# Kernel optimization log

Hardware: AMD Instinct MI355X
Metric: run time of the kernel (lower is better)

The kernel has to match this reference:

```python
import jax, jax.numpy as jnp
import numpy as np

B, S_IN, T_OUT, H, L, V = 64, 512, 64, 1024, 2, 1024


def setup_inputs() -> dict:
    key = jax.random.key(0)
    ks = iter(jax.random.split(key, 64))
    def p(shape, scale=0.02):
        return (jax.random.normal(next(ks), shape, jnp.float32) * scale)
    d = {"x": jax.random.normal(next(ks), (B, 2, S_IN), jnp.float32)}
    d["emb"] = p((V, H))
    for l in range(L):
        i = 2 if l == 0 else H
        d[f"enc_Wih{l}"] = p((3 * H, i)); d[f"enc_Whh{l}"] = p((3 * H, H))
        d[f"enc_bih{l}"] = p((3 * H,));   d[f"enc_bhh{l}"] = p((3 * H,))
        d[f"dec_Wih{l}"] = p((H, H));     d[f"dec_Whh{l}"] = p((H, H))
        d[f"dec_bih{l}"] = p((H,));       d[f"dec_bhh{l}"] = p((H,))
    d["hq_W"] = p((H, H)); d["hq_b"] = p((H,))
    d["comb_W"] = p((H, 2 * H)); d["comb_b"] = p((H,))
    d["fc_W"] = p((V, H)); d["fc_b"] = p((V,))
    return d


def _gru_layer(x_seq, Wih, Whh, bih, bhh):
    # x_seq: [B,T,I] -> (outputs [B,T,H], h_T [B,H]). PyTorch GRU gate order r,z,n.
    xp = jnp.einsum('bti,gi->btg', x_seq, Wih) + bih  # [B,T,3H]
    h0 = jnp.zeros((x_seq.shape[0], Whh.shape[1]), x_seq.dtype)
    def step(h, xpt):
        hp = h @ Whh.T + bhh
        xr, xz, xn = jnp.split(xpt, 3, axis=-1)
        hr, hz, hn = jnp.split(hp, 3, axis=-1)
        r = jax.nn.sigmoid(xr + hr)
        z = jax.nn.sigmoid(xz + hz)
        n = jnp.tanh(xn + r * hn)
        h = (1.0 - z) * n + z * h
        return h, h
    hT, ys = jax.lax.scan(step, h0, jnp.swapaxes(xp, 0, 1))
    return jnp.swapaxes(ys, 0, 1), hT


def _forward(x, emb,
             enc_Wih0, enc_Whh0, enc_bih0, enc_bhh0,
             enc_Wih1, enc_Whh1, enc_bih1, enc_bhh1,
             dec_Wih0, dec_Whh0, dec_bih0, dec_bhh0,
             dec_Wih1, dec_Whh1, dec_bih1, dec_bhh1,
             hq_W, hq_b, comb_W, comb_b, fc_W, fc_b):
    enc_params = [(enc_Wih0, enc_Whh0, enc_bih0, enc_bhh0),
                  (enc_Wih1, enc_Whh1, enc_bih1, enc_bhh1)]
    dec_params = [(dec_Wih0, dec_Whh0, dec_bih0, dec_bhh0),
                  (dec_Wih1, dec_Whh1, dec_bih1, dec_bhh1)]
    # ---- encoder: GRU over x permuted to [B, S_in, 2] ----
    seq = jnp.transpose(x, (0, 2, 1)).astype(jnp.float32)
    h_enc = []
    for (Wih, Whh, bih, bhh) in enc_params:
        seq, hT = _gru_layer(seq, Wih, Whh, bih, bhh)
        h_enc.append(hT)
    enc_outs = seq                      # [B, S_in, H]
    hidden0 = jnp.stack(h_enc, axis=0)  # [L, B, H]

    tok0 = jnp.zeros((B,), jnp.int32)
    def dec_step(carry, _):
        tok, hid = carry
        inp = emb[tok]                  # [B, H]
        new_h = []
        for l, (Wih, Whh, bih, bhh) in enumerate(dec_params):
            h = jnp.tanh(inp @ Wih.T + bih + hid[l] @ Whh.T + bhh)
            new_h.append(h)
            inp = h
        hid = jnp.stack(new_h, axis=0)
        q = inp @ hq_W.T + hq_b                          # [B, H]
        scores = jnp.einsum('bsh,bh->bs', enc_outs, q)   # [B, S_in]
        aw = jax.nn.softmax(scores, axis=1)
        att = jnp.einsum('bs,bsh->bh', aw, enc_outs)     # [B, H]
        logits = jnp.concatenate([inp, att], axis=-1) @ comb_W.T + comb_b
        logits = logits @ fc_W.T + fc_b                  # [B, V]
        tok = jnp.argmax(logits, axis=-1).astype(jnp.int32)
        return (tok, hid), (logits, aw)
    (_, hidden), (logits_t, aw_t) = jax.lax.scan(dec_step, (tok0, hidden0), None, length=T_OUT)
    vec_out = jnp.swapaxes(logits_t, 0, 1)   # [B, T_out, V]
    attn = aw_t[-1][:, None, :]              # [B, 1, S_in] (last step, as in source)
    return vec_out, hidden, attn


def reference(x, emb,
              enc_Wih0, enc_Whh0, enc_bih0, enc_bhh0,
              enc_Wih1, enc_Whh1, enc_bih1, enc_bhh1,
              dec_Wih0, dec_Whh0, dec_bih0, dec_bhh0,
              dec_Wih1, dec_Whh1, dec_bih1, dec_bhh1,
              hq_W, hq_b, comb_W, comb_b, fc_W, fc_b):
    return _forward(x, emb,
                    enc_Wih0, enc_Whh0, enc_bih0, enc_bhh0,
                    enc_Wih1, enc_Whh1, enc_bih1, enc_bhh1,
                    dec_Wih0, dec_Whh0, dec_bih0, dec_bhh0,
                    dec_Wih1, dec_Whh1, dec_bih1, dec_bhh1,
                    hq_W, hq_b, comb_W, comb_b, fc_W, fc_b)
```

## Files before the change

kernel.cpp:

```cpp
#include <hip/hip_runtime.h>
#include <stdint.h>


#define BB 64
#define SS 512
#define TT 64
#define HH 1024
#define VV 1024
#define BH 65536
#define SH 524288
#define OFF_HID  4194304
#define OFF_ATTN 4325376

typedef _Float16 half8  __attribute__((ext_vector_type(8)));
typedef float    floatx4 __attribute__((ext_vector_type(4)));

struct P {
  const float *x, *emb;
  const float *eWih0, *eWhh0, *ebih0, *ebhh0;
  const float *dWih0, *dWhh0, *dbih0, *dbhh0;
  const float *eWih1, *eWhh1, *ebih1, *ebhh1;
  const float *dWih1, *dWhh1, *dbih1, *dbhh1;
  const float *hqW, *hqb, *combW, *combb, *fcW, *fcb;
  uint32_t* enc_i;
  _Float16 *W0h,*W0l;
  _Float16 *W1h,*W1l;
  _Float16 *embh,*embl,*T0h,*T0l;
  _Float16 *wih0dh,*wih0dl,*wih1dh,*wih1dl,*whh0dh,*whh0dl,*whh1dh,*whh1dl;
  _Float16 *hqh,*hql,*combh,*combl,*fch,*fcl;
  _Float16 *h0h,*h0l,*h1h,*h1l;
  _Float16 *dh0h,*dh0l,*dh1h,*dh1l;
  _Float16 *cath,*catl;
  _Float16 *ch,*cl;
  float *u0,*u1,*w1x,*q;
  float *attp_o;
  float *attp_ml;
  float *sc63;
  unsigned long long* amax;
  float* dout;
};

struct GSet { const _Float16 *Wh, *Wl, *Ah, *Al; const float *bias; float *out; };

__device__ __forceinline__ void splitf(float x, _Float16& hi, _Float16& lo){
  _Float16 h = (_Float16)x; hi = h;
  lo = (_Float16)((x - (float)h) * 2048.0f);
}
__device__ __forceinline__ float reconf(_Float16 hi, _Float16 lo){
  return fmaf((float)lo, 1.0f/2048.0f, (float)hi);
}
__device__ __forceinline__ float recon_u32(uint32_t w){
  float hi = (float)__builtin_bit_cast(_Float16, (unsigned short)(w & 0xffffu));
  float lo = (float)__builtin_bit_cast(_Float16, (unsigned short)(w >> 16));
  return fmaf(lo, 1.0f/2048.0f, hi);
}
__device__ __forceinline__ uint32_t pack_pair(float x){
  _Float16 hi, lo; splitf(x, hi, lo);
  return (uint32_t)__builtin_bit_cast(unsigned short, hi)
       | ((uint32_t)__builtin_bit_cast(unsigned short, lo) << 16);
}
__device__ __forceinline__ unsigned ordf(float f){
  unsigned u = __float_as_uint(f);
  return (u & 0x80000000u) ? ~u : (u | 0x80000000u);
}

template<int NT, int KH, bool SPLIT>
__device__ __forceinline__ void gemm_core(
    const _Float16* __restrict__ Ah0, const _Float16* __restrict__ Al0,
    const _Float16* __restrict__ Ah1, const _Float16* __restrict__ Al1,
    int sA,
    const _Float16* __restrict__ Wh, const _Float16* __restrict__ Wl,
    int nrows, _Float16* ldsW, float* accOut)
{
  const int tid = threadIdx.x, lane = tid & 63, wave = tid >> 6;
  const int mA = (wave<<4) + (lane & 15);
  const int kb = ((lane>>4) << 3);
  const int wstride = KH << 10;
  floatx4 aH[NT], aM1[NT], aM2[NT];
  int ne[NT];
  const _Float16* bh_base[NT];
  const _Float16* bl_base[NT];
  #pragma unroll
  for (int nt=0; nt<NT; ++nt){
    int nn = (lane & 15) + (nt<<4);
    ne[nt] = nn < nrows ? nn : nrows - 1;
    bh_base[nt] = ldsW + ne[nt]*1032 + kb;
    aH[nt]  = floatx4{0.f,0.f,0.f,0.f};
    aM1[nt] = floatx4{0.f,0.f,0.f,0.f};
    aM2[nt] = floatx4{0.f,0.f,0.f,0.f};
  }
  #pragma unroll
  for (int kh=0; kh<KH; ++kh){
    __syncthreads();
    const int iters = (nrows*128 + 255) >> 8;
    for (int it=0; it<iters; ++it){
      int idx = tid + (it<<8);
      int row = idx >> 7, col = (idx & 127) << 3;
      if (row < nrows)
        *(half8*)(ldsW + row*1032 + col) =
            *(const half8*)(Wh + row*wstride + (kh<<10) + col);
    }
    __syncthreads();
    const _Float16* ah_p = ((KH==2 && kh==1) ? Ah1 : Ah0) + mA*sA + kb;
    const _Float16* al_p = ((KH==2 && kh==1) ? Al1 : Al0) + mA*sA + kb;
    #pragma unroll
    for (int nt=0; nt<NT; ++nt) bl_base[nt] = Wl + ne[nt]*wstride + (kh<<10) + kb;
    #pragma unroll 4
    for (int ks=0; ks<32; ++ks){
      half8 ah = *(const half8*)(ah_p + (ks<<5));
      half8 al = *(const half8*)(al_p + (ks<<5));
      #pragma unroll
      for (int nt=0; nt<NT; ++nt){
        half8 bh = *(const half8*)(bh_base[nt] + (ks<<5));
        half8 bl = *(const half8*)(bl_base[nt] + (ks<<5));
        aH[nt]  = __builtin_amdgcn_mfma_f32_16x16x32_f16(ah, bh, aH[nt],  0,0,0);
        aM1[nt] = __builtin_amdgcn_mfma_f32_16x16x32_f16(ah, bl, aM1[nt], 0,0,0);
        aM2[nt] = __builtin_amdgcn_mfma_f32_16x16x32_f16(al, bh, aM2[nt], 0,0,0);
      }
    }
    if (SPLIT){
      #pragma unroll
      for (int nt=0; nt<NT; ++nt){
        #pragma unroll
        for (int r=0;r<4;++r)
          accOut[(kh*NT + nt)*4 + r] = aH[nt][r] + (aM1[nt][r] + aM2[nt][r]) * (1.f/2048.f);
        aH[nt]  = floatx4{0.f,0.f,0.f,0.f};
        aM1[nt] = floatx4{0.f,0.f,0.f,0.f};
        aM2[nt] = floatx4{0.f,0.f,0.f,0.f};
      }
    }
  }
  if (!SPLIT){
    #pragma unroll
    for (int nt=0; nt<NT; ++nt)
      #pragma unroll
      for (int r=0;r<4;++r)
        accOut[nt*4 + r] = aH[nt][r] + (aM1[nt][r] + aM2[nt][r]) * (1.f/2048.f);
  }
}

__global__ __launch_bounds__(256) void k_split(const float* __restrict__ src,
                                               _Float16* dh, _Float16* dl, int n){
  for (int i = blockIdx.x*256 + threadIdx.x; i < n; i += gridDim.x*256){
    _Float16 hi,lo; splitf(src[i],hi,lo); dh[i]=hi; dl[i]=lo;
  }
}

__global__ __launch_bounds__(256) void k_rw0(P p){
  const int n = 128*24*1024;
  for (int i = blockIdx.x*256 + threadIdx.x; i < n; i += gridDim.x*256){
    int k = i & 1023; int rest = i >> 10; int rr = rest % 24; int blk = rest / 24;
    int grow = (rr>>3)*1024 + (blk<<3) + (rr&7);
    _Float16 hi,lo; splitf(p.eWhh0[grow*1024 + k],hi,lo);
    p.W0h[i]=hi; p.W0l[i]=lo;
  }
}
__global__ __launch_bounds__(256) void k_rw1(P p){
  const int n = 128*24*2048;
  for (int i = blockIdx.x*256 + threadIdx.x; i < n; i += gridDim.x*256){
    int k = i & 2047; int rest = i >> 11; int rr = rest % 24; int blk = rest / 24;
    int grow = (rr>>3)*1024 + (blk<<3) + (rr&7);
    float v = (k < 1024) ? p.eWhh1[grow*1024 + k] : p.eWih1[grow*1024 + (k-1024)];
    _Float16 hi,lo; splitf(v,hi,lo);
    p.W1h[i]=hi; p.W1l[i]=lo;
  }
}
__global__ __launch_bounds__(256) void k_zero(P p){
  int i = blockIdx.x*256 + threadIdx.x;
  p.h1h[i] = (_Float16)0.f; p.h1l[i] = (_Float16)0.f;
  p.h0h[BH + i] = (_Float16)0.f; p.h0l[BH + i] = (_Float16)0.f;
}
__global__ __launch_bounds__(256) void k_t0(P p){
  __shared__ _Float16 ldsW[16*1032];
  const int ns = blockIdx.x & 63, mc = blockIdx.x >> 6;
  float acc[4];
  gemm_core<1,1,false>(p.embh + mc*65536, p.embl + mc*65536, nullptr, nullptr, 1024,
                       p.wih0dh + ns*16*1024, p.wih0dl + ns*16*1024, 16, ldsW, acc);
  const int lane = threadIdx.x & 63, wave = threadIdx.x >> 6;
  const int n = lane & 15, col = (ns<<4) + n;
  const float bv = p.dbih0[col];
  #pragma unroll
  for (int r=0;r<4;++r){
    int v = mc*64 + (wave<<4) + ((lane>>4)<<2) + r;
    _Float16 hi,lo; splitf(acc[r] + bv, hi, lo);
    p.T0h[v*1024 + col] = hi; p.T0l[v*1024 + col] = lo;
  }
}

__global__ __launch_bounds__(256) void k_enc(P p, int e){
  const int tid = threadIdx.x, lane = tid & 63, wave = tid >> 6;
  const bool is0 = blockIdx.x < 128;
  if (is0 && e >= 512) return;
  if (!is0 && e < 1) return;
  const int blk = is0 ? blockIdx.x : blockIdx.x - 128;
  const int j0 = blk << 3;

  __shared__ _Float16 ldsW[24*1032];
  __shared__ float ldsG[2][24][68];
  __shared__ float ldsC[24][4];

  if (tid < 24){
    int grow = (tid>>3)*1024 + j0 + (tid & 7);
    if (is0){
      ldsC[tid][0] = p.eWih0[grow*2+0];
      ldsC[tid][1] = p.eWih0[grow*2+1];
      ldsC[tid][2] = p.ebih0[grow];
      ldsC[tid][3] = p.ebhh0[grow];
    } else {
      ldsC[tid][0] = p.ebih1[grow];
      ldsC[tid][1] = p.ebhh1[grow];
    }
  }

  const int cur = e & 1, prv = cur ^ 1;
  float acc[16];
  if (is0){
    gemm_core<2,1,true>(p.h0h + prv*BH, p.h0l + prv*BH, nullptr, nullptr, 1024,
                        p.W0h + blk*24*1024, p.W0l + blk*24*1024, 24, ldsW, acc);
    #pragma unroll
    for (int nt=0; nt<2; ++nt){
      int n = (lane & 15) + (nt<<4);
      if (n < 24){
        #pragma unroll
        for (int r=0;r<4;++r)
          ldsG[0][n][(wave<<4)+((lane>>4)<<2)+r] = acc[nt*4+r];
      }
    }
  } else {
    gemm_core<2,2,true>(p.h1h + prv*BH, p.h1l + prv*BH,
                        p.h0h + prv*BH, p.h0l + prv*BH, 1024,
                        p.W1h + blk*24*2048, p.W1l + blk*24*2048, 24, ldsW, acc);
    #pragma unroll
    for (int kh=0; kh<2; ++kh){
      #pragma unroll
      for (int nt=0; nt<2; ++nt){
        int n = (lane & 15) + (nt<<4);
        if (n < 24){
          #pragma unroll
          for (int r=0;r<4;++r)
            ldsG[kh][n][(wave<<4)+((lane>>4)<<2)+r] = acc[(kh*2+nt)*4+r];
        }
      }
    }
  }
  __syncthreads();

  #pragma unroll
  for (int it=0; it<2; ++it){
    int idx = tid + (it<<8);
    int b = idx & 63, j = idx >> 6;
    int col = j0 + j;
    if (is0){
      int t = e;
      float hr = ldsG[0][j][b]    + ldsC[j][3];
      float hz = ldsG[0][8+j][b]  + ldsC[8+j][3];
      float hn = ldsG[0][16+j][b] + ldsC[16+j][3];
      float x0 = p.x[b*1024 + t], x1 = p.x[b*1024 + 512 + t];
      float xr = fmaf(x0, ldsC[j][0],    fmaf(x1, ldsC[j][1],    ldsC[j][2]));
      float xz = fmaf(x0, ldsC[8+j][0],  fmaf(x1, ldsC[8+j][1],  ldsC[8+j][2]));
      float xn = fmaf(x0, ldsC[16+j][0], fmaf(x1, ldsC[16+j][1], ldsC[16+j][2]));
      float rg = 1.0f/(1.0f + expf(-(xr+hr)));
      float zg = 1.0f/(1.0f + expf(-(xz+hz)));
      float ng = tanhf(xn + rg*hn);
      float hold = reconf(p.h0h[prv*BH + b*1024 + col], p.h0l[prv*BH + b*1024 + col]);
      float hnew = (1.0f - zg)*ng + zg*hold;
      _Float16 hi,lo; splitf(hnew,hi,lo);
      p.h0h[cur*BH + b*1024 + col] = hi;
      p.h0l[cur*BH + b*1024 + col] = lo;
    } else {
      int t = e - 1;
      float hr = ldsG[0][j][b]    + ldsC[j][1];
      float hz = ldsG[0][8+j][b]  + ldsC[8+j][1];
      float hn = ldsG[0][16+j][b] + ldsC[16+j][1];
      float xr = ldsG[1][j][b]    + ldsC[j][0];
      float xz = ldsG[1][8+j][b]  + ldsC[8+j][0];
      float xn = ldsG[1][16+j][b] + ldsC[16+j][0];
      float rg = 1.0f/(1.0f + expf(-(xr+hr)));
      float zg = 1.0f/(1.0f + expf(-(xz+hz)));
      float ng = tanhf(xn + rg*hn);
      float hold = reconf(p.h1h[prv*BH + b*1024 + col], p.h1l[prv*BH + b*1024 + col]);
      float hnew = (1.0f - zg)*ng + zg*hold;
      _Float16 hi,lo; splitf(hnew,hi,lo);
      p.h1h[cur*BH + b*1024 + col] = hi;
      p.h1l[cur*BH + b*1024 + col] = lo;
      p.enc_i[b*SH + t*1024 + col] = pack_pair(hnew);
    }
  }
}

__global__ __launch_bounds__(256) void k_dgemm2(GSet a, GSet b){
  const int tid = threadIdx.x, lane = tid & 63, wave = tid >> 6;
  const GSet g = blockIdx.x < 128 ? a : b;
  const int blk = blockIdx.x & 127;
  __shared__ _Float16 ldsW[8*1032];
  float acc[4];
  gemm_core<1,1,false>(g.Ah, g.Al, nullptr, nullptr, 1024,
                       g.Wh + blk*8*1024, g.Wl + blk*8*1024, 8, ldsW, acc);
  int n = lane & 15;
  if (n < 8){
    int col = (blk<<3) + n;
    float bv = g.bias[col];
    #pragma unroll
    for (int r=0;r<4;++r){
      int m = (wave<<4)+((lane>>4)<<2)+r;
      g.out[m*1024 + col] = acc[r] + bv;
    }
  }
}

__global__ __launch_bounds__(256) void k_dec0(P p, int t){
  const int tid = threadIdx.x, b = blockIdx.x;
  __shared__ unsigned long long red[256];
  unsigned long long v = 0;
  if (t > 0 && tid < 128) v = p.amax[b*128 + tid];
  red[tid] = v; __syncthreads();
  for (int off=128; off>=1; off>>=1){
    if (tid < off){ unsigned long long o = red[tid+off]; if (o > red[tid]) red[tid] = o; }
    __syncthreads();
  }
  const int tokb = (t > 0) ? (1023 - (int)(red[0] & 0xffffffffULL)) : 0;
  #pragma unroll
  for (int i=0;i<4;++i){
    int h = tid + (i<<8);
    float val = tanhf(reconf(p.T0h[tokb*1024+h], p.T0l[tokb*1024+h]) + p.u0[b*1024+h]);
    _Float16 hi,lo; splitf(val,hi,lo);
    p.dh0h[b*1024+h]=hi; p.dh0l[b*1024+h]=lo;
  }
}
__global__ __launch_bounds__(256) void k_dec2(P p){
  const int tid = threadIdx.x, b = blockIdx.x;
  #pragma unroll
  for (int i=0;i<4;++i){
    int h = tid + (i<<8);
    float val = tanhf(p.w1x[b*1024+h] + p.u1[b*1024+h]);
    _Float16 hi,lo; splitf(val,hi,lo);
    p.dh1h[b*1024+h]=hi; p.dh1l[b*1024+h]=lo;
    p.cath[b*2048+h]=hi; p.catl[b*2048+h]=lo;
  }
}
__global__ __launch_bounds__(256) void k_flash(P p, int t){
  const int tid = threadIdx.x, lane = tid & 63, wave = tid >> 6;
  const int b = blockIdx.x >> 1, half = blockIdx.x & 1;
  const int s0 = half << 8;
  const bool last = (t == 63);
  float qv[16];
  #pragma unroll
  for (int i=0;i<16;++i) qv[i] = p.q[b*1024 + (i<<6) + lane];
  float ov[16];
  #pragma unroll
  for (int i=0;i<16;++i) ov[i] = 0.f;
  float mrun = -3.0e38f, lrun = 0.f;
  for (int si=0; si<64; ++si){
    int s = s0 + (wave<<6) + si;
    const uint32_t* ep = p.enc_i + b*SH + s*1024 + lane;
    float ef[16]; float partial = 0.f;
    #pragma unroll
    for (int i=0;i<16;++i){
      ef[i] = recon_u32(ep[i<<6]);
      partial = fmaf(ef[i], qv[i], partial);
    }
    #pragma unroll
    for (int off=32; off; off>>=1) partial += __shfl_xor(partial, off, 64);
    if (last && lane == 0) p.sc63[b*512 + s] = partial;
    float mnew = fmaxf(mrun, partial);
    float fac = __expf(mrun - mnew);
    float w   = __expf(partial - mnew);
    lrun = fmaf(lrun, fac, w);
    #pragma unroll
    for (int i=0;i<16;++i) ov[i] = fmaf(ov[i], fac, w*ef[i]);
    mrun = mnew;
  }
  __shared__ float ldsO[4][1024];
  __shared__ float ldsM[4], ldsL2[4];
  #pragma unroll
  for (int i=0;i<16;++i) ldsO[wave][(i<<6)+lane] = ov[i];
  if (lane == 0){ ldsM[wave] = mrun; ldsL2[wave] = lrun; }
  __syncthreads();
  float M = fmaxf(fmaxf(ldsM[0],ldsM[1]), fmaxf(ldsM[2],ldsM[3]));
  float f0 = __expf(ldsM[0]-M), f1 = __expf(ldsM[1]-M),
        f2 = __expf(ldsM[2]-M), f3 = __expf(ldsM[3]-M);
  if (tid == 0){
    p.attp_ml[b*4 + half*2 + 0] = M;
    p.attp_ml[b*4 + half*2 + 1] = f0*ldsL2[0] + f1*ldsL2[1] + f2*ldsL2[2] + f3*ldsL2[3];
  }
  #pragma unroll
  for (int i=0;i<4;++i){
    int h = tid + (i<<8);
    p.attp_o[(b*2+half)*1024 + h] =
        f0*ldsO[0][h] + f1*ldsO[1][h] + f2*ldsO[2][h] + f3*ldsO[3][h];
  }
}
__global__ __launch_bounds__(256) void k_dec5(P p, int t){
  const int tid = threadIdx.x, b = blockIdx.x;
  float m0 = p.attp_ml[b*4+0], l0 = p.attp_ml[b*4+1];
  float m1 = p.attp_ml[b*4+2], l1 = p.attp_ml[b*4+3];
  float M = fmaxf(m0,m1);
  float f0 = expf(m0-M), f1 = expf(m1-M);
  float invL = 1.0f/(f0*l0 + f1*l1);
  #pragma unroll
  for (int i=0;i<4;++i){
    int h = tid + (i<<8);
    float o = (f0*p.attp_o[(b*2+0)*1024+h] + f1*p.attp_o[(b*2+1)*1024+h]) * invL;
    _Float16 hi,lo; splitf(o,hi,lo);
    p.cath[b*2048 + 1024 + h] = hi; p.catl[b*2048 + 1024 + h] = lo;
  }
  if (t == 63){
    #pragma unroll
    for (int i=0;i<2;++i){
      int s = tid + (i<<8);
      p.dout[OFF_ATTN + b*512 + s] = expf(p.sc63[b*512+s] - M) * invL;
    }
  }
}
__global__ __launch_bounds__(256) void k_comb(P p){
  const int tid = threadIdx.x, lane = tid & 63, wave = tid >> 6;
  const int blk = blockIdx.x;
  __shared__ _Float16 ldsW[8*1032];
  float acc[4];
  gemm_core<1,2,false>(p.cath, p.catl, p.cath + 1024, p.catl + 1024, 2048,
                       p.combh + blk*8*2048, p.combl + blk*8*2048, 8, ldsW, acc);
  int n = lane & 15;
  if (n < 8){
    int col = (blk<<3) + n;
    float bv = p.combb[col];
    #pragma unroll
    for (int r=0;r<4;++r){
      int m = (wave<<4)+((lane>>4)<<2)+r;
      _Float16 hi,lo; splitf(acc[r] + bv, hi, lo);
      p.ch[m*1024 + col] = hi; p.cl[m*1024 + col] = lo;
    }
  }
}
__global__ __launch_bounds__(256) void k_fc(P p, int t){
  const int tid = threadIdx.x, lane = tid & 63, wave = tid >> 6;
  const int blk = blockIdx.x;
  __shared__ _Float16 ldsW[8*1032];
  __shared__ float ldsL[8][68];
  float acc[4];
  gemm_core<1,1,false>(p.ch, p.cl, nullptr, nullptr, 1024,
                       p.fch + blk*8*1024, p.fcl + blk*8*1024, 8, ldsW, acc);
  int n = lane & 15;
  if (n < 8){
    int col = (blk<<3) + n;
    float bv = p.fcb[col];
    #pragma unroll
    for (int r=0;r<4;++r){
      int m = (wave<<4)+((lane>>4)<<2)+r;
      float val = acc[r] + bv;
      p.dout[m*65536 + t*1024 + col] = val;
      ldsL[n][m] = val;
    }
  }
  __syncthreads();
  if (tid < 64){
    int b = tid; float best = -3.0e38f; int bi = 0;
    #pragma unroll
    for (int jj=0; jj<8; ++jj){
      float v = ldsL[jj][b];
      if (v > best){ best = v; bi = jj; }
    }
    unsigned long long pk = ((unsigned long long)ordf(best) << 32)
                          | (unsigned)(1023 - ((blk<<3) + bi));
    p.amax[b*128 + blk] = pk;
  }
}
__global__ __launch_bounds__(256) void k_hidden(P p){
  int idx = blockIdx.x*256 + threadIdx.x;
  int i = idx & 65535;
  float v = (idx >> 16) ? reconf(p.dh1h[i], p.dh1l[i]) : reconf(p.dh0h[i], p.dh0l[i]);
  p.dout[OFF_HID + idx] = v;
}

extern "C" void kernel_launch(void* const* d_in, const int* in_sizes, int n_in,
                              void* d_out, int out_size, void* d_ws, size_t ws_size,
                              hipStream_t stream)
{
  (void)in_sizes; (void)n_in; (void)out_size;
  P p;
  p.x     = (const float*)d_in[0];  p.emb   = (const float*)d_in[1];
  p.eWih0 = (const float*)d_in[2];  p.eWhh0 = (const float*)d_in[3];
  p.ebih0 = (const float*)d_in[4];  p.ebhh0 = (const float*)d_in[5];
  p.dWih0 = (const float*)d_in[6];  p.dWhh0 = (const float*)d_in[7];
  p.dbih0 = (const float*)d_in[8];  p.dbhh0 = (const float*)d_in[9];
  p.eWih1 = (const float*)d_in[10]; p.eWhh1 = (const float*)d_in[11];
  p.ebih1 = (const float*)d_in[12]; p.ebhh1 = (const float*)d_in[13];
  p.dWih1 = (const float*)d_in[14]; p.dWhh1 = (const float*)d_in[15];
  p.dbih1 = (const float*)d_in[16]; p.dbhh1 = (const float*)d_in[17];
  p.hqW   = (const float*)d_in[18]; p.hqb   = (const float*)d_in[19];
  p.combW = (const float*)d_in[20]; p.combb = (const float*)d_in[21];
  p.fcW   = (const float*)d_in[22]; p.fcb   = (const float*)d_in[23];
  p.dout  = (float*)d_out;

  char* base = (char*)d_ws; size_t off = 0;
  auto alloc = [&](size_t bytes)->char*{
    char* r = base + off; off = (off + bytes + 255) & ~(size_t)255; return r;
  };
  p.enc_i = (uint32_t*)alloc(33554432ULL*4);
  p.W0h = (_Float16*)alloc(3145728ULL*2);  p.W0l = (_Float16*)alloc(3145728ULL*2);
  p.W1h = (_Float16*)alloc(6291456ULL*2);  p.W1l = (_Float16*)alloc(6291456ULL*2);
  p.embh = (_Float16*)alloc(1048576ULL*2); p.embl = (_Float16*)alloc(1048576ULL*2);
  p.T0h  = (_Float16*)alloc(1048576ULL*2); p.T0l  = (_Float16*)alloc(1048576ULL*2);
  p.wih0dh=(_Float16*)alloc(1048576ULL*2); p.wih0dl=(_Float16*)alloc(1048576ULL*2);
  p.wih1dh=(_Float16*)alloc(1048576ULL*2); p.wih1dl=(_Float16*)alloc(1048576ULL*2);
  p.whh0dh=(_Float16*)alloc(1048576ULL*2); p.whh0dl=(_Float16*)alloc(1048576ULL*2);
  p.whh1dh=(_Float16*)alloc(1048576ULL*2); p.whh1dl=(_Float16*)alloc(1048576ULL*2);
  p.hqh  = (_Float16*)alloc(1048576ULL*2); p.hql  = (_Float16*)alloc(1048576ULL*2);
  p.combh= (_Float16*)alloc(2097152ULL*2); p.combl= (_Float16*)alloc(2097152ULL*2);
  p.fch  = (_Float16*)alloc(1048576ULL*2); p.fcl  = (_Float16*)alloc(1048576ULL*2);
  p.h0h  = (_Float16*)alloc(131072ULL*2);  p.h0l  = (_Float16*)alloc(131072ULL*2);
  p.h1h  = (_Float16*)alloc(131072ULL*2);  p.h1l  = (_Float16*)alloc(131072ULL*2);
  p.dh0h = (_Float16*)alloc(65536ULL*2);   p.dh0l = (_Float16*)alloc(65536ULL*2);
  p.dh1h = (_Float16*)alloc(65536ULL*2);   p.dh1l = (_Float16*)alloc(65536ULL*2);
  p.cath = (_Float16*)alloc(131072ULL*2);  p.catl = (_Float16*)alloc(131072ULL*2);
  p.ch   = (_Float16*)alloc(65536ULL*2);   p.cl   = (_Float16*)alloc(65536ULL*2);
  p.u0   = (float*)alloc(65536ULL*4);      p.u1   = (float*)alloc(65536ULL*4);
  p.w1x  = (float*)alloc(65536ULL*4);      p.q    = (float*)alloc(65536ULL*4);
  p.attp_o  = (float*)alloc(131072ULL*4);
  p.attp_ml = (float*)alloc(256ULL*4);
  p.sc63    = (float*)alloc(32768ULL*4);
  p.amax    = (unsigned long long*)alloc(8192ULL*8);
  if (off > ws_size) return;

  k_split<<<2048,256,0,stream>>>(p.emb,   p.embh,   p.embl,   1048576);
  k_split<<<2048,256,0,stream>>>(p.dWih0, p.wih0dh, p.wih0dl, 1048576);
  k_split<<<2048,256,0,stream>>>(p.dWih1, p.wih1dh, p.wih1dl, 1048576);
  k_split<<<2048,256,0,stream>>>(p.dWhh0, p.whh0dh, p.whh0dl, 1048576);
  k_split<<<2048,256,0,stream>>>(p.dWhh1, p.whh1dh, p.whh1dl, 1048576);
  k_split<<<2048,256,0,stream>>>(p.hqW,   p.hqh,    p.hql,    1048576);
  k_split<<<2048,256,0,stream>>>(p.combW, p.combh,  p.combl,  2097152);
  k_split<<<2048,256,0,stream>>>(p.fcW,   p.fch,    p.fcl,    1048576);
  k_rw0<<<4096,256,0,stream>>>(p);
  k_rw1<<<4096,256,0,stream>>>(p);
  k_zero<<<256,256,0,stream>>>(p);
  k_t0<<<1024,256,0,stream>>>(p);

  for (int e=0; e<=512; ++e) k_enc<<<256,256,0,stream>>>(p, e);

  {
    GSet a{p.whh0dh, p.whh0dl, p.h0h + BH, p.h0l + BH, p.dbhh0, p.u0};
    GSet b{p.whh1dh, p.whh1dl, p.h1h,      p.h1l,      p.dbhh1, p.u1};
    k_dgemm2<<<256,256,0,stream>>>(a, b);
  }
  GSet sK1a{p.wih1dh, p.wih1dl, p.dh0h, p.dh0l, p.dbih1, p.w1x};
  GSet sK1b{p.whh0dh, p.whh0dl, p.dh0h, p.dh0l, p.dbhh0, p.u0};
  GSet sK3a{p.hqh,    p.hql,    p.dh1h, p.dh1l, p.hqb,   p.q};
  GSet sK3b{p.whh1dh, p.whh1dl, p.dh1h, p.dh1l, p.dbhh1, p.u1};

  for (int t=0; t<64; ++t){
    k_dec0<<<64,256,0,stream>>>(p, t);
    k_dgemm2<<<256,256,0,stream>>>(sK1a, sK1b);
    k_dec2<<<64,256,0,stream>>>(p);
    k_dgemm2<<<256,256,0,stream>>>(sK3a, sK3b);
    k_flash<<<128,256,0,stream>>>(p, t);
    k_dec5<<<64,256,0,stream>>>(p, t);
    k_comb<<<128,256,0,stream>>>(p);
    k_fc<<<128,256,0,stream>>>(p, t);
  }
  k_hidden<<<512,256,0,stream>>>(p);
}
```

Measured before the change: 30.20 ms.

## Convert encoder and decoder step loops into persistent kernels with grid barriers

```diff
diff --git a/kernel.cpp b/kernel.cpp
--- a/kernel.cpp
+++ b/kernel.cpp
@@ -12,8 +12,13 @@
 #define OFF_HID  4194304
 #define OFF_ATTN 4325376
 
+#define ENC_LDS 158304
+#define DEC_LDS 137472
+
 typedef _Float16 half8  __attribute__((ext_vector_type(8)));
 typedef float    floatx4 __attribute__((ext_vector_type(4)));
+
+#define MFMA16(a,b,c) __builtin_amdgcn_mfma_f32_16x16x32_f16(a,b,c,0,0,0)
 
 struct P {
   const float *x, *emb;
@@ -22,25 +27,21 @@
   const float *eWih1, *eWhh1, *ebih1, *ebhh1;
   const float *dWih1, *dWhh1, *dbih1, *dbhh1;
   const float *hqW, *hqb, *combW, *combb, *fcW, *fcb;
-  uint32_t* enc_i;
-  _Float16 *W0h,*W0l;
-  _Float16 *W1h,*W1l;
+  uint32_t* enc_att;
   _Float16 *embh,*embl,*T0h,*T0l;
-  _Float16 *wih0dh,*wih0dl,*wih1dh,*wih1dl,*whh0dh,*whh0dl,*whh1dh,*whh1dl;
-  _Float16 *hqh,*hql,*combh,*combl,*fch,*fcl;
+  _Float16 *wih0dh,*wih0dl;
   _Float16 *h0h,*h0l,*h1h,*h1l;
   _Float16 *dh0h,*dh0l,*dh1h,*dh1l;
   _Float16 *cath,*catl;
   _Float16 *ch,*cl;
-  float *u0,*u1,*w1x,*q;
+  float *u0,*u1,*q;
   float *attp_o;
   float *attp_ml;
   float *sc63;
   unsigned long long* amax;
+  unsigned *bar0, *bar1;
   float* dout;
 };
-
-struct GSet { const _Float16 *Wh, *Wl, *Ah, *Al; const float *bias; float *out; };
 
 __device__ __forceinline__ void splitf(float x, _Float16& hi, _Float16& lo){
   _Float16 h = (_Float16)x; hi = h;
@@ -49,19 +50,43 @@
 __device__ __forceinline__ float reconf(_Float16 hi, _Float16 lo){
   return fmaf((float)lo, 1.0f/2048.0f, (float)hi);
 }
-__device__ __forceinline__ float recon_u32(uint32_t w){
-  float hi = (float)__builtin_bit_cast(_Float16, (unsigned short)(w & 0xffffu));
-  float lo = (float)__builtin_bit_cast(_Float16, (unsigned short)(w >> 16));
-  return fmaf(lo, 1.0f/2048.0f, hi);
-}
-__device__ __forceinline__ uint32_t pack_pair(float x){
-  _Float16 hi, lo; splitf(x, hi, lo);
-  return (uint32_t)__builtin_bit_cast(unsigned short, hi)
-       | ((uint32_t)__builtin_bit_cast(unsigned short, lo) << 16);
-}
 __device__ __forceinline__ unsigned ordf(float f){
   unsigned u = __float_as_uint(f);
   return (u & 0x80000000u) ? ~u : (u | 0x80000000u);
+}
+__device__ __forceinline__ void pack2(float v0, float v1, uint32_t& ph, uint32_t& pl){
+  _Float16 h0,l0,h1,l1; splitf(v0,h0,l0); splitf(v1,h1,l1);
+  ph = (uint32_t)__builtin_bit_cast(unsigned short,h0)
+     | ((uint32_t)__builtin_bit_cast(unsigned short,h1) << 16);
+  pl = (uint32_t)__builtin_bit_cast(unsigned short,l0)
+     | ((uint32_t)__builtin_bit_cast(unsigned short,l1) << 16);
+}
+__device__ __forceinline__ void st_u32(uint32_t* p2, uint32_t v){
+  __hip_atomic_store(p2, v, __ATOMIC_RELAXED, __HIP_MEMORY_SCOPE_SYSTEM);
+}
+__device__ __forceinline__ void st_f32(float* p2, float v){
+  __hip_atomic_store(p2, v, __ATOMIC_RELAXED, __HIP_MEMORY_SCOPE_SYSTEM);
+}
+__device__ __forceinline__ void st_u64(unsigned long long* p2, unsigned long long v){
+  __hip_atomic_store(p2, v, __ATOMIC_RELAXED, __HIP_MEMORY_SCOPE_SYSTEM);
+}
+
+__device__ __forceinline__ void gbar(unsigned* c, unsigned target){
+  __syncthreads();
+  if (threadIdx.x == 0){
+    __hip_atomic_fetch_add(c + (blockIdx.x & 3)*64, 1u,
+                           __ATOMIC_RELEASE, __HIP_MEMORY_SCOPE_SYSTEM);
+    unsigned s;
+    do {
+      __builtin_amdgcn_s_sleep(2);
+      s = __hip_atomic_load(c,       __ATOMIC_RELAXED, __HIP_MEMORY_SCOPE_SYSTEM)
+        + __hip_atomic_load(c + 64,  __ATOMIC_RELAXED, __HIP_MEMORY_SCOPE_SYSTEM)
+        + __hip_atomic_load(c + 128, __ATOMIC_RELAXED, __HIP_MEMORY_SCOPE_SYSTEM)
+        + __hip_atomic_load(c + 192, __ATOMIC_RELAXED, __HIP_MEMORY_SCOPE_SYSTEM);
+    } while (s < target);
+  }
+  __syncthreads();
+  __builtin_amdgcn_fence(__ATOMIC_ACQUIRE, "agent");
 }
 
 template<int NT, int KH, bool SPLIT>
@@ -113,30 +138,17 @@
       for (int nt=0; nt<NT; ++nt){
         half8 bh = *(const half8*)(bh_base[nt] + (ks<<5));
         half8 bl = *(const half8*)(bl_base[nt] + (ks<<5));
-        aH[nt]  = __builtin_amdgcn_mfma_f32_16x16x32_f16(ah, bh, aH[nt],  0,0,0);
-        aM1[nt] = __builtin_amdgcn_mfma_f32_16x16x32_f16(ah, bl, aM1[nt], 0,0,0);
-        aM2[nt] = __builtin_amdgcn_mfma_f32_16x16x32_f16(al, bh, aM2[nt], 0,0,0);
-      }
-    }
-    if (SPLIT){
-      #pragma unroll
-      for (int nt=0; nt<NT; ++nt){
-        #pragma unroll
-        for (int r=0;r<4;++r)
-          accOut[(kh*NT + nt)*4 + r] = aH[nt][r] + (aM1[nt][r] + aM2[nt][r]) * (1.f/2048.f);
-        aH[nt]  = floatx4{0.f,0.f,0.f,0.f};
-        aM1[nt] = floatx4{0.f,0.f,0.f,0.f};
-        aM2[nt] = floatx4{0.f,0.f,0.f,0.f};
-      }
-    }
-  }
-  if (!SPLIT){
+        aH[nt]  = MFMA16(ah, bh, aH[nt]);
+        aM1[nt] = MFMA16(ah, bl, aM1[nt]);
+        aM2[nt] = MFMA16(al, bh, aM2[nt]);
+      }
+    }
+  }
+  #pragma unroll
+  for (int nt=0; nt<NT; ++nt)
     #pragma unroll
-    for (int nt=0; nt<NT; ++nt)
-      #pragma unroll
-      for (int r=0;r<4;++r)
-        accOut[nt*4 + r] = aH[nt][r] + (aM1[nt][r] + aM2[nt][r]) * (1.f/2048.f);
-  }
+    for (int r=0;r<4;++r)
+      accOut[nt*4 + r] = aH[nt][r] + (aM1[nt][r] + aM2[nt][r]) * (1.f/2048.f);
 }
 
 __global__ __launch_bounds__(256) void k_split(const float* __restrict__ src,
@@ -145,30 +157,11 @@
     _Float16 hi,lo; splitf(src[i],hi,lo); dh[i]=hi; dl[i]=lo;
   }
 }
-
-__global__ __launch_bounds__(256) void k_rw0(P p){
-  const int n = 128*24*1024;
-  for (int i = blockIdx.x*256 + threadIdx.x; i < n; i += gridDim.x*256){
-    int k = i & 1023; int rest = i >> 10; int rr = rest % 24; int blk = rest / 24;
-    int grow = (rr>>3)*1024 + (blk<<3) + (rr&7);
-    _Float16 hi,lo; splitf(p.eWhh0[grow*1024 + k],hi,lo);
-    p.W0h[i]=hi; p.W0l[i]=lo;
-  }
-}
-__global__ __launch_bounds__(256) void k_rw1(P p){
-  const int n = 128*24*2048;
-  for (int i = blockIdx.x*256 + threadIdx.x; i < n; i += gridDim.x*256){
-    int k = i & 2047; int rest = i >> 11; int rr = rest % 24; int blk = rest / 24;
-    int grow = (rr>>3)*1024 + (blk<<3) + (rr&7);
-    float v = (k < 1024) ? p.eWhh1[grow*1024 + k] : p.eWih1[grow*1024 + (k-1024)];
-    _Float16 hi,lo; splitf(v,hi,lo);
-    p.W1h[i]=hi; p.W1l[i]=lo;
-  }
-}
 __global__ __launch_bounds__(256) void k_zero(P p){
   int i = blockIdx.x*256 + threadIdx.x;
   p.h1h[i] = (_Float16)0.f; p.h1l[i] = (_Float16)0.f;
   p.h0h[BH + i] = (_Float16)0.f; p.h0l[BH + i] = (_Float16)0.f;
+  if (i < 512) p.bar0[i] = 0u;
 }
 __global__ __launch_bounds__(256) void k_t0(P p){
   __shared__ _Float16 ldsW[16*1032];
@@ -187,288 +180,467 @@
   }
 }
 
-__global__ __launch_bounds__(256) void k_enc(P p, int e){
+__global__ __launch_bounds__(512,1) void k_encp(P p){
+  extern __shared__ char smem[];
+  _Float16* W0h = (_Float16*)smem;
+  _Float16* W0l = W0h + 12384;
+  _Float16* W1h = W0l + 12384;
+  _Float16* W1l = W1h + 24672;
+  float* ldsA = (float*)(smem + 148224);
+  float* ldsC = ldsA + 2448;
   const int tid = threadIdx.x, lane = tid & 63, wave = tid >> 6;
-  const bool is0 = blockIdx.x < 128;
-  if (is0 && e >= 512) return;
-  if (!is0 && e < 1) return;
-  const int blk = is0 ? blockIdx.x : blockIdx.x - 128;
-  const int j0 = blk << 3;
-
-  __shared__ _Float16 ldsW[24*1032];
-  __shared__ float ldsG[2][24][68];
-  __shared__ float ldsC[24][4];
-
-  if (tid < 24){
-    int grow = (tid>>3)*1024 + j0 + (tid & 7);
-    if (is0){
-      ldsC[tid][0] = p.eWih0[grow*2+0];
-      ldsC[tid][1] = p.eWih0[grow*2+1];
-      ldsC[tid][2] = p.ebih0[grow];
-      ldsC[tid][3] = p.ebhh0[grow];
-    } else {
-      ldsC[tid][0] = p.ebih1[grow];
-      ldsC[tid][1] = p.ebhh1[grow];
-    }
-  }
-
-  const int cur = e & 1, prv = cur ^ 1;
-  float acc[16];
-  if (is0){
-    gemm_core<2,1,true>(p.h0h + prv*BH, p.h0l + prv*BH, nullptr, nullptr, 1024,
-                        p.W0h + blk*24*1024, p.W0l + blk*24*1024, 24, ldsW, acc);
-    #pragma unroll
-    for (int nt=0; nt<2; ++nt){
-      int n = (lane & 15) + (nt<<4);
-      if (n < 24){
-        #pragma unroll
-        for (int r=0;r<4;++r)
-          ldsG[0][n][(wave<<4)+((lane>>4)<<2)+r] = acc[nt*4+r];
-      }
-    }
-  } else {
-    gemm_core<2,2,true>(p.h1h + prv*BH, p.h1l + prv*BH,
-                        p.h0h + prv*BH, p.h0l + prv*BH, 1024,
-                        p.W1h + blk*24*2048, p.W1l + blk*24*2048, 24, ldsW, acc);
-    #pragma unroll
-    for (int kh=0; kh<2; ++kh){
-      #pragma unroll
-      for (int nt=0; nt<2; ++nt){
-        int n = (lane & 15) + (nt<<4);
-        if (n < 24){
+  const int bid = blockIdx.x, j0 = bid << 2;
+
+  for (int idx=tid; idx<12*1024; idx+=512){
+    int r=idx>>10, k=idx&1023;
+    int grow=(r>>2)*1024 + j0 + (r&3);
+    _Float16 hi,lo; splitf(p.eWhh0[grow*1024+k],hi,lo);
+    W0h[r*1032+k]=hi; W0l[r*1032+k]=lo;
+  }
+  for (int idx=tid; idx<12*2048; idx+=512){
+    int r=idx>>11, k=idx&2047;
+    int grow=(r>>2)*1024 + j0 + (r&3);
+    float v = (k<1024)? p.eWhh1[grow*1024+k] : p.eWih1[grow*1024+(k-1024)];
+    _Float16 hi,lo; splitf(v,hi,lo);
+    W1h[r*2056+k]=hi; W1l[r*2056+k]=lo;
+  }
+  if (tid<12){
+    int grow=(tid>>2)*1024 + j0 + (tid&3);
+    ldsC[tid*6+0]=p.eWih0[grow*2+0]; ldsC[tid*6+1]=p.eWih0[grow*2+1];
+    ldsC[tid*6+2]=p.ebih0[grow];     ldsC[tid*6+3]=p.ebhh0[grow];
+    ldsC[tid*6+4]=p.ebih1[grow];     ldsC[tid*6+5]=p.ebhh1[grow];
+  }
+  __syncthreads();
+
+  const int ln15 = lane & 15, kb = (lane >> 4) << 3;
+  const bool isl1 = wave >= 4;
+  const int mt = wave & 3;
+  const int brow = (ln15 < 12) ? ln15 : 11;
+  const int mrow = (mt<<4) + ln15;
+  const int msub = (mt<<4) + ((lane>>4)<<2);
+
+  #pragma unroll 1
+  for (int e=0; e<=512; ++e){
+    const int cur=e&1, prv=cur^1;
+    if (!isl1){
+      if (e < 512){
+        const _Float16* ah = p.h0h + prv*BH + mrow*1024 + kb;
+        const _Float16* al = p.h0l + prv*BH + mrow*1024 + kb;
+        const _Float16* bh = W0h + brow*1032 + kb;
+        const _Float16* bl = W0l + brow*1032 + kb;
+        floatx4 H{0,0,0,0},M{0,0,0,0},N{0,0,0,0};
+        #pragma unroll 8
+        for (int ks=0;ks<32;++ks){
+          int off=ks<<5;
+          half8 A=*(const half8*)(ah+off), Alo=*(const half8*)(al+off);
+          half8 B=*(const half8*)(bh+off), Blo=*(const half8*)(bl+off);
+          H=MFMA16(A,B,H); M=MFMA16(A,Blo,M); N=MFMA16(Alo,B,N);
+        }
+        if (ln15<12){
           #pragma unroll
           for (int r=0;r<4;++r)
-            ldsG[kh][n][(wave<<4)+((lane>>4)<<2)+r] = acc[(kh*2+nt)*4+r];
-        }
-      }
+            ldsA[ln15*68 + msub + r] = H[r] + (M[r]+N[r])*(1.f/2048.f);
+        }
+      }
+    } else {
+      if (e >= 1){
+        const _Float16* a1h = p.h1h + prv*BH + mrow*1024 + kb;
+        const _Float16* a1l = p.h1l + prv*BH + mrow*1024 + kb;
+        const _Float16* a0h = p.h0h + prv*BH + mrow*1024 + kb;
+        const _Float16* a0l = p.h0l + prv*BH + mrow*1024 + kb;
+        const _Float16* bh = W1h + brow*2056 + kb;
+        const _Float16* bl = W1l + brow*2056 + kb;
+        floatx4 H1{0,0,0,0},M1{0,0,0,0},N1{0,0,0,0};
+        floatx4 H2{0,0,0,0},M2{0,0,0,0},N2{0,0,0,0};
+        #pragma unroll 8
+        for (int ks=0;ks<32;++ks){
+          int off=ks<<5;
+          half8 A=*(const half8*)(a1h+off), Alo=*(const half8*)(a1l+off);
+          half8 B=*(const half8*)(bh+off), Blo=*(const half8*)(bl+off);
+          H1=MFMA16(A,B,H1); M1=MFMA16(A,Blo,M1); N1=MFMA16(Alo,B,N1);
+        }
+        #pragma unroll 8
+        for (int ks=0;ks<32;++ks){
+          int off=ks<<5;
+          half8 A=*(const half8*)(a0h+off), Alo=*(const half8*)(a0l+off);
+          half8 B=*(const half8*)(bh+1024+off), Blo=*(const half8*)(bl+1024+off);
+          H2=MFMA16(A,B,H2); M2=MFMA16(A,Blo,M2); N2=MFMA16(Alo,B,N2);
+        }
+        if (ln15<12){
+          #pragma unroll
+          for (int r=0;r<4;++r){
+            ldsA[(12+ln15)*68 + msub + r] = H1[r] + (M1[r]+N1[r])*(1.f/2048.f);
+            ldsA[(24+ln15)*68 + msub + r] = H2[r] + (M2[r]+N2[r])*(1.f/2048.f);
+          }
+        }
+      }
+    }
+    __syncthreads();
+    if (tid < 256){
+      const bool l1t = tid >= 128;
+      const int b = tid & 63, jp = (tid>>6) & 1;
+      const int c0 = j0 + (jp<<1);
+      if (!l1t && e < 512){
+        const float x0 = p.x[b*1024+e], x1 = p.x[b*1024+512+e];
+        float nv[2];
+        #pragma unroll
+        for (int d=0; d<2; ++d){
+          int jj=(jp<<1)+d, r0=jj, r1=4+jj, r2=8+jj;
+          float hr = ldsA[r0*68+b] + ldsC[r0*6+3];
+          float hz = ldsA[r1*68+b] + ldsC[r1*6+3];
+          float hn = ldsA[r2*68+b] + ldsC[r2*6+3];
+          float xr = fmaf(x0, ldsC[r0*6+0], fmaf(x1, ldsC[r0*6+1], ldsC[r0*6+2]));
+          float xz = fmaf(x0, ldsC[r1*6+0], fmaf(x1, ldsC[r1*6+1], ldsC[r1*6+2]));
+          float xn = fmaf(x0, ldsC[r2*6+0], fmaf(x1, ldsC[r2*6+1], ldsC[r2*6+2]));
+          float rg = 1.0f/(1.0f + expf(-(xr+hr)));
+          float zg = 1.0f/(1.0f + expf(-(xz+hz)));
+          float ng = tanhf(xn + rg*hn);
+          float hold = reconf(p.h0h[prv*BH + b*1024 + c0+d], p.h0l[prv*BH + b*1024 + c0+d]);
+          nv[d] = (1.0f - zg)*ng + zg*hold;
+        }
+        uint32_t ph_,pl_; pack2(nv[0],nv[1],ph_,pl_);
+        st_u32((uint32_t*)(p.h0h + cur*BH) + ((b*1024+c0)>>1), ph_);
+        st_u32((uint32_t*)(p.h0l + cur*BH) + ((b*1024+c0)>>1), pl_);
+      } else if (l1t && e >= 1){
+        const int t = e-1;
+        float nv[2];
+        #pragma unroll
+        for (int d=0; d<2; ++d){
+          int jj=(jp<<1)+d, r0=jj, r1=4+jj, r2=8+jj;
+          float hr = ldsA[(12+r0)*68+b] + ldsC[r0*6+5];
+          float hz = ldsA[(12+r1)*68+b] + ldsC[r1*6+5];
+          float hn = ldsA[(12+r2)*68+b] + ldsC[r2*6+5];
+          float xr = ldsA[(24+r0)*68+b] + ldsC[r0*6+4];
+          float xz = ldsA[(24+r1)*68+b] + ldsC[r1*6+4];
+          float xn = ldsA[(24+r2)*68+b] + ldsC[r2*6+4];
+          float rg = 1.0f/(1.0f + expf(-(xr+hr)));
+          float zg = 1.0f/(1.0f + expf(-(xz+hz)));
+          float ng = tanhf(xn + rg*hn);
+          float hold = reconf(p.h1h[prv*BH + b*1024 + c0+d], p.h1l[prv*BH + b*1024 + c0+d]);
+          nv[d] = (1.0f - zg)*ng + zg*hold;
+        }
+        uint32_t ph_,pl_; pack2(nv[0],nv[1],ph_,pl_);
+        st_u32((uint32_t*)(p.h1h + cur*BH) + ((b*1024+c0)>>1), ph_);
+        st_u32((uint32_t*)(p.h1l + cur*BH) + ((b*1024+c0)>>1), pl_);
+        _Float16 e0=(_Float16)nv[0], e1=(_Float16)nv[1];
+        uint32_t pe = (uint32_t)__builtin_bit_cast(unsigned short,e0)
+                    | ((uint32_t)__builtin_bit_cast(unsigned short,e1) << 16);
+        st_u32(p.enc_att + (((size_t)b*SH + t*1024 + c0)>>1), pe);
+      }
+    }
+    gbar(p.bar0, (unsigned)(e+1) << 8);
+  }
+}
+
+__device__ __forceinline__ void dmm_dual(int lane, int wave,
+    const _Float16* A0h, const _Float16* A0l,
+    const _Float16* A1h, const _Float16* A1l,
+    const _Float16* W0h_, const _Float16* W0l_,
+    const _Float16* W1h_, const _Float16* W1l_,
+    float* ldsD)
+{
+  const int mt = wave>>1, sel = wave&1;
+  const int ln15 = lane&15, kb = (lane>>4)<<3, n = ln15&3;
+  const _Float16* ah = (sel? A1h:A0h) + ((mt<<4)+ln15)*1024 + kb;
+  const _Float16* al = (sel? A1l:A0l) + ((mt<<4)+ln15)*1024 + kb;
+  const _Float16* bh = (sel? W1h_:W0h_) + n*1032 + kb;
+  const _Float16* bl = (sel? W1l_:W0l_) + n*1032 + kb;
+  floatx4 H{0,0,0,0},M{0,0,0,0},N{0,0,0,0};
+  #pragma unroll 8
+  for (int ks=0;ks<32;++ks){
+    int off=ks<<5;
+    half8 A=*(const half8*)(ah+off), Alo=*(const half8*)(al+off);
+    half8 B=*(const half8*)(bh+off), Blo=*(const half8*)(bl+off);
+    H=MFMA16(A,B,H); M=MFMA16(A,Blo,M); N=MFMA16(Alo,B,N);
+  }
+  if (ln15 < 4){
+    #pragma unroll
+    for (int r=0;r<4;++r)
+      ldsD[sel*272 + n*68 + (mt<<4)+((lane>>4)<<2)+r] = H[r]+(M[r]+N[r])*(1.f/2048.f);
+  }
+}
+template<int K>
+__device__ __forceinline__ void dmm_sk(int lane, int wave,
+    const _Float16* Ah, const _Float16* Al,
+    const _Float16* Wh_, const _Float16* Wl_,
+    float* ldsD)
+{
+  const int mt = wave>>1, kg = wave&1;
+  const int ln15 = lane&15, kb = (lane>>4)<<3, n = ln15&3;
+  const int k0 = kg*(K/2);
+  const _Float16* ah = Ah + ((mt<<4)+ln15)*K + k0 + kb;
+  const _Float16* al = Al + ((mt<<4)+ln15)*K + k0 + kb;
+  const _Float16* bh = Wh_ + n*(K+8) + k0 + kb;
+  const _Float16* bl = Wl_ + n*(K+8) + k0 + kb;
+  floatx4 H{0,0,0,0},M{0,0,0,0},N{0,0,0,0};
+  #pragma unroll 8
+  for (int ks=0;ks<K/64;++ks){
+    int off=ks<<5;
+    half8 A=*(const half8*)(ah+off), Alo=*(const half8*)(al+off);
+    half8 B=*(const half8*)(bh+off), Blo=*(const half8*)(bl+off);
+    H=MFMA16(A,B,H); M=MFMA16(A,Blo,M); N=MFMA16(Alo,B,N);
+  }
+  if (ln15 < 4){
+    #pragma unroll
+    for (int r=0;r<4;++r)
+      ldsD[kg*272 + n*68 + (mt<<4)+((lane>>4)<<2)+r] = H[r]+(M[r]+N[r])*(1.f/2048.f);
+  }
+}
+
+__global__ __launch_bounds__(512,1) void k_decp(P p){
+  extern __shared__ char smem[];
+  _Float16* wih1h=(_Float16*)smem;      _Float16* wih1l=wih1h+4128;
+  _Float16* whh0h=wih1l+4128;           _Float16* whh0l=whh0h+4128;
+  _Float16* hqh2 =whh0l+4128;           _Float16* hql2 =hqh2+4128;
+  _Float16* whh1h=hql2+4128;            _Float16* whh1l=whh1h+4128;
+  _Float16* fch2 =whh1l+4128;           _Float16* fcl2 =fch2+4128;
+  _Float16* combh2=fcl2+4128;           _Float16* combl2=combh2+8224;
+  float* sbufA=(float*)(smem+115456);
+  float* ldsD =(float*)(smem+131968);
+  float* ldsL =(float*)(smem+134144);
+  float* sml  =(float*)(smem+135232);
+  float* cb   =(float*)(smem+135296);
+  unsigned long long* sred=(unsigned long long*)(smem+135424);
+
+  const int tid=threadIdx.x, lane=tid&63, wave=tid>>6;
+  const int bid=blockIdx.x, j0=bid<<2;
+
+  { const float* mats[5]={p.dWih1,p.dWhh0,p.hqW,p.dWhh1,p.fcW};
+    _Float16* mh[5]={wih1h,whh0h,hqh2,whh1h,fch2};
+    _Float16* ml[5]={wih1l,whh0l,hql2,whh1l,fcl2};
+    #pragma unroll 1
+    for (int m5=0;m5<5;++m5)
+      for (int idx=tid; idx<4096; idx+=512){
+        int r=idx>>10,k=idx&1023;
+        _Float16 hi,lo; splitf(mats[m5][(j0+r)*1024+k],hi,lo);
+        mh[m5][r*1032+k]=hi; ml[m5][r*1032+k]=lo;
+      }
+    for (int idx=tid; idx<8192; idx+=512){
+      int r=idx>>11,k=idx&2047;
+      _Float16 hi,lo; splitf(p.combW[(j0+r)*2048+k],hi,lo);
+      combh2[r*2056+k]=hi; combl2[r*2056+k]=lo;
+    }
+    if (tid<4){
+      cb[0*4+tid]=p.dbih1[j0+tid]; cb[1*4+tid]=p.dbhh0[j0+tid];
+      cb[2*4+tid]=p.hqb[j0+tid];   cb[3*4+tid]=p.dbhh1[j0+tid];
+      cb[4*4+tid]=p.combb[j0+tid]; cb[5*4+tid]=p.fcb[j0+tid];
     }
   }
   __syncthreads();
-
-  #pragma unroll
-  for (int it=0; it<2; ++it){
-    int idx = tid + (it<<8);
-    int b = idx & 63, j = idx >> 6;
-    int col = j0 + j;
-    if (is0){
-      int t = e;
-      float hr = ldsG[0][j][b]    + ldsC[j][3];
-      float hz = ldsG[0][8+j][b]  + ldsC[8+j][3];
-      float hn = ldsG[0][16+j][b] + ldsC[16+j][3];
-      float x0 = p.x[b*1024 + t], x1 = p.x[b*1024 + 512 + t];
-      float xr = fmaf(x0, ldsC[j][0],    fmaf(x1, ldsC[j][1],    ldsC[j][2]));
-      float xz = fmaf(x0, ldsC[8+j][0],  fmaf(x1, ldsC[8+j][1],  ldsC[8+j][2]));
-      float xn = fmaf(x0, ldsC[16+j][0], fmaf(x1, ldsC[16+j][1], ldsC[16+j][2]));
-      float rg = 1.0f/(1.0f + expf(-(xr+hr)));
-      float zg = 1.0f/(1.0f + expf(-(xz+hz)));
-      float ng = tanhf(xn + rg*hn);
-      float hold = reconf(p.h0h[prv*BH + b*1024 + col], p.h0l[prv*BH + b*1024 + col]);
-      float hnew = (1.0f - zg)*ng + zg*hold;
-      _Float16 hi,lo; splitf(hnew,hi,lo);
-      p.h0h[cur*BH + b*1024 + col] = hi;
-      p.h0l[cur*BH + b*1024 + col] = lo;
-    } else {
-      int t = e - 1;
-      float hr = ldsG[0][j][b]    + ldsC[j][1];
-      float hz = ldsG[0][8+j][b]  + ldsC[8+j][1];
-      float hn = ldsG[0][16+j][b] + ldsC[16+j][1];
-      float xr = ldsG[1][j][b]    + ldsC[j][0];
-      float xz = ldsG[1][8+j][b]  + ldsC[8+j][0];
-      float xn = ldsG[1][16+j][b] + ldsC[16+j][0];
-      float rg = 1.0f/(1.0f + expf(-(xr+hr)));
-      float zg = 1.0f/(1.0f + expf(-(xz+hz)));
-      float ng = tanhf(xn + rg*hn);
-      float hold = reconf(p.h1h[prv*BH + b*1024 + col], p.h1l[prv*BH + b*1024 + col]);
-      float hnew = (1.0f - zg)*ng + zg*hold;
-      _Float16 hi,lo; splitf(hnew,hi,lo);
-      p.h1h[cur*BH + b*1024 + col] = hi;
-      p.h1l[cur*BH + b*1024 + col] = lo;
-      p.enc_i[b*SH + t*1024 + col] = pack_pair(hnew);
-    }
-  }
-}
-
-__global__ __launch_bounds__(256) void k_dgemm2(GSet a, GSet b){
-  const int tid = threadIdx.x, lane = tid & 63, wave = tid >> 6;
-  const GSet g = blockIdx.x < 128 ? a : b;
-  const int blk = blockIdx.x & 127;
-  __shared__ _Float16 ldsW[8*1032];
-  float acc[4];
-  gemm_core<1,1,false>(g.Ah, g.Al, nullptr, nullptr, 1024,
-                       g.Wh + blk*8*1024, g.Wl + blk*8*1024, 8, ldsW, acc);
-  int n = lane & 15;
-  if (n < 8){
-    int col = (blk<<3) + n;
-    float bv = g.bias[col];
-    #pragma unroll
-    for (int r=0;r<4;++r){
-      int m = (wave<<4)+((lane>>4)<<2)+r;
-      g.out[m*1024 + col] = acc[r] + bv;
-    }
-  }
-}
-
-__global__ __launch_bounds__(256) void k_dec0(P p, int t){
-  const int tid = threadIdx.x, b = blockIdx.x;
-  __shared__ unsigned long long red[256];
-  unsigned long long v = 0;
-  if (t > 0 && tid < 128) v = p.amax[b*128 + tid];
-  red[tid] = v; __syncthreads();
-  for (int off=128; off>=1; off>>=1){
-    if (tid < off){ unsigned long long o = red[tid+off]; if (o > red[tid]) red[tid] = o; }
+  unsigned phx = 0;
+
+  dmm_dual(lane,wave, p.h0h+BH,p.h0l+BH, p.h1h,p.h1l,
+           whh0h,whh0l, whh1h,whh1l, ldsD);
+  __syncthreads();
+  if (tid<256){
+    int b=tid&63, j=tid>>6, col=j0+j;
+    st_f32(p.u0 + b*1024+col, ldsD[j*68+b]     + cb[1*4+j]);
+    st_f32(p.u1 + b*1024+col, ldsD[272+j*68+b] + cb[3*4+j]);
+  }
+  ++phx; gbar(p.bar1, phx<<8);
+
+  #pragma unroll 1
+  for (int t=0; t<64; ++t){
+    if (bid < 64){
+      const int b = bid;
+      if (tid<256){
+        unsigned long long v=0;
+        if (t>0) v = p.amax[b*256+tid];
+        sred[tid]=v;
+      }
+      __syncthreads();
+      for (int o=128;o>=1;o>>=1){
+        if (tid<o){ unsigned long long x=sred[tid+o]; if (x>sred[tid]) sred[tid]=x; }
+        __syncthreads();
+      }
+      const int tok = (t>0)? (1023 - (int)(sred[0]&0xffffffffULL)) : 0;
+      int h2=tid<<1;
+      float v0=tanhf(reconf(p.T0h[tok*1024+h2],  p.T0l[tok*1024+h2])   + p.u0[b*1024+h2]);
+      float v1=tanhf(reconf(p.T0h[tok*1024+h2+1],p.T0l[tok*1024+h2+1]) + p.u0[b*1024+h2+1]);
+      uint32_t ph_,pl_; pack2(v0,v1,ph_,pl_);
+      st_u32((uint32_t*)p.dh0h + ((b*1024+h2)>>1), ph_);
+      st_u32((uint32_t*)p.dh0l + ((b*1024+h2)>>1), pl_);
+    }
+    ++phx; gbar(p.bar1, phx<<8);
+
+    dmm_dual(lane,wave, p.dh0h,p.dh0l, p.dh0h,p.dh0l,
+             wih1h,wih1l, whh0h,whh0l, ldsD);
     __syncthreads();
-  }
-  const int tokb = (t > 0) ? (1023 - (int)(red[0] & 0xffffffffULL)) : 0;
-  #pragma unroll
-  for (int i=0;i<4;++i){
-    int h = tid + (i<<8);
-    float val = tanhf(reconf(p.T0h[tokb*1024+h], p.T0l[tokb*1024+h]) + p.u0[b*1024+h]);
-    _Float16 hi,lo; splitf(val,hi,lo);
-    p.dh0h[b*1024+h]=hi; p.dh0l[b*1024+h]=lo;
-  }
-}
-__global__ __launch_bounds__(256) void k_dec2(P p){
-  const int tid = threadIdx.x, b = blockIdx.x;
-  #pragma unroll
-  for (int i=0;i<4;++i){
-    int h = tid + (i<<8);
-    float val = tanhf(p.w1x[b*1024+h] + p.u1[b*1024+h]);
-    _Float16 hi,lo; splitf(val,hi,lo);
-    p.dh1h[b*1024+h]=hi; p.dh1l[b*1024+h]=lo;
-    p.cath[b*2048+h]=hi; p.catl[b*2048+h]=lo;
-  }
-}
-__global__ __launch_bounds__(256) void k_flash(P p, int t){
-  const int tid = threadIdx.x, lane = tid & 63, wave = tid >> 6;
-  const int b = blockIdx.x >> 1, half = blockIdx.x & 1;
-  const int s0 = half << 8;
-  const bool last = (t == 63);
-  float qv[16];
-  #pragma unroll
-  for (int i=0;i<16;++i) qv[i] = p.q[b*1024 + (i<<6) + lane];
-  float ov[16];
-  #pragma unroll
-  for (int i=0;i<16;++i) ov[i] = 0.f;
-  float mrun = -3.0e38f, lrun = 0.f;
-  for (int si=0; si<64; ++si){
-    int s = s0 + (wave<<6) + si;
-    const uint32_t* ep = p.enc_i + b*SH + s*1024 + lane;
-    float ef[16]; float partial = 0.f;
-    #pragma unroll
-    for (int i=0;i<16;++i){
-      ef[i] = recon_u32(ep[i<<6]);
-      partial = fmaf(ef[i], qv[i], partial);
-    }
-    #pragma unroll
-    for (int off=32; off; off>>=1) partial += __shfl_xor(partial, off, 64);
-    if (last && lane == 0) p.sc63[b*512 + s] = partial;
-    float mnew = fmaxf(mrun, partial);
-    float fac = __expf(mrun - mnew);
-    float w   = __expf(partial - mnew);
-    lrun = fmaf(lrun, fac, w);
-    #pragma unroll
-    for (int i=0;i<16;++i) ov[i] = fmaf(ov[i], fac, w*ef[i]);
-    mrun = mnew;
-  }
-  __shared__ float ldsO[4][1024];
-  __shared__ float ldsM[4], ldsL2[4];
-  #pragma unroll
-  for (int i=0;i<16;++i) ldsO[wave][(i<<6)+lane] = ov[i];
-  if (lane == 0){ ldsM[wave] = mrun; ldsL2[wave] = lrun; }
-  __syncthreads();
-  float M = fmaxf(fmaxf(ldsM[0],ldsM[1]), fmaxf(ldsM[2],ldsM[3]));
-  float f0 = __expf(ldsM[0]-M), f1 = __expf(ldsM[1]-M),
-        f2 = __expf(ldsM[2]-M), f3 = __expf(ldsM[3]-M);
-  if (tid == 0){
-    p.attp_ml[b*4 + half*2 + 0] = M;
-    p.attp_ml[b*4 + half*2 + 1] = f0*ldsL2[0] + f1*ldsL2[1] + f2*ldsL2[2] + f3*ldsL2[3];
-  }
-  #pragma unroll
-  for (int i=0;i<4;++i){
-    int h = tid + (i<<8);
-    p.attp_o[(b*2+half)*1024 + h] =
-        f0*ldsO[0][h] + f1*ldsO[1][h] + f2*ldsO[2][h] + f3*ldsO[3][h];
-  }
-}
-__global__ __launch_bounds__(256) void k_dec5(P p, int t){
-  const int tid = threadIdx.x, b = blockIdx.x;
-  float m0 = p.attp_ml[b*4+0], l0 = p.attp_ml[b*4+1];
-  float m1 = p.attp_ml[b*4+2], l1 = p.attp_ml[b*4+3];
-  float M = fmaxf(m0,m1);
-  float f0 = expf(m0-M), f1 = expf(m1-M);
-  float invL = 1.0f/(f0*l0 + f1*l1);
-  #pragma unroll
-  for (int i=0;i<4;++i){
-    int h = tid + (i<<8);
-    float o = (f0*p.attp_o[(b*2+0)*1024+h] + f1*p.attp_o[(b*2+1)*1024+h]) * invL;
-    _Float16 hi,lo; splitf(o,hi,lo);
-    p.cath[b*2048 + 1024 + h] = hi; p.catl[b*2048 + 1024 + h] = lo;
-  }
-  if (t == 63){
-    #pragma unroll
-    for (int i=0;i<2;++i){
-      int s = tid + (i<<8);
-      p.dout[OFF_ATTN + b*512 + s] = expf(p.sc63[b*512+s] - M) * invL;
-    }
-  }
-}
-__global__ __launch_bounds__(256) void k_comb(P p){
-  const int tid = threadIdx.x, lane = tid & 63, wave = tid >> 6;
-  const int blk = blockIdx.x;
-  __shared__ _Float16 ldsW[8*1032];
-  float acc[4];
-  gemm_core<1,2,false>(p.cath, p.catl, p.cath + 1024, p.catl + 1024, 2048,
-                       p.combh + blk*8*2048, p.combl + blk*8*2048, 8, ldsW, acc);
-  int n = lane & 15;
-  if (n < 8){
-    int col = (blk<<3) + n;
-    float bv = p.combb[col];
-    #pragma unroll
-    for (int r=0;r<4;++r){
-      int m = (wave<<4)+((lane>>4)<<2)+r;
-      _Float16 hi,lo; splitf(acc[r] + bv, hi, lo);
-      p.ch[m*1024 + col] = hi; p.cl[m*1024 + col] = lo;
-    }
-  }
-}
-__global__ __launch_bounds__(256) void k_fc(P p, int t){
-  const int tid = threadIdx.x, lane = tid & 63, wave = tid >> 6;
-  const int blk = blockIdx.x;
-  __shared__ _Float16 ldsW[8*1032];
-  __shared__ float ldsL[8][68];
-  float acc[4];
-  gemm_core<1,1,false>(p.ch, p.cl, nullptr, nullptr, 1024,
-                       p.fch + blk*8*1024, p.fcl + blk*8*1024, 8, ldsW, acc);
-  int n = lane & 15;
-  if (n < 8){
-    int col = (blk<<3) + n;
-    float bv = p.fcb[col];
-    #pragma unroll
-    for (int r=0;r<4;++r){
-      int m = (wave<<4)+((lane>>4)<<2)+r;
-      float val = acc[r] + bv;
-      p.dout[m*65536 + t*1024 + col] = val;
-      ldsL[n][m] = val;
-    }
-  }
-  __syncthreads();
-  if (tid < 64){
-    int b = tid; float best = -3.0e38f; int bi = 0;
-    #pragma unroll
-    for (int jj=0; jj<8; ++jj){
-      float v = ldsL[jj][b];
-      if (v > best){ best = v; bi = jj; }
-    }
-    unsigned long long pk = ((unsigned long long)ordf(best) << 32)
-                          | (unsigned)(1023 - ((blk<<3) + bi));
-    p.amax[b*128 + blk] = pk;
-  }
-}
-__global__ __launch_bounds__(256) void k_hidden(P p){
-  int idx = blockIdx.x*256 + threadIdx.x;
-  int i = idx & 65535;
-  float v = (idx >> 16) ? reconf(p.dh1h[i], p.dh1l[i]) : reconf(p.dh0h[i], p.dh0l[i]);
-  p.dout[OFF_HID + idx] = v;
+    if (tid<128){
+      int b=tid&63, jp=tid>>6;
+      float nv[2];
+      #pragma unroll
+      for (int d=0;d<2;++d){
+        int j=(jp<<1)+d, col=j0+j;
+        nv[d] = tanhf(ldsD[j*68+b] + cb[0*4+j] + p.u1[b*1024+col]);
+      }
+      uint32_t ph_,pl_; pack2(nv[0],nv[1],ph_,pl_);
+      int c0=j0+(jp<<1);
+      st_u32((uint32_t*)p.dh1h + ((b*1024+c0)>>1), ph_);
+      st_u32((uint32_t*)p.dh1l + ((b*1024+c0)>>1), pl_);
+      st_u32((uint32_t*)p.cath + ((b*2048+c0)>>1), ph_);
+      st_u32((uint32_t*)p.catl + ((b*2048+c0)>>1), pl_);
+    } else if (tid<256){
+      int t2=tid-128; int b=t2&63, jp=t2>>6;
+      #pragma unroll
+      for (int d=0;d<2;++d){
+        int j=(jp<<1)+d, col=j0+j;
+        st_f32(p.u0 + b*1024+col, ldsD[272+j*68+b] + cb[1*4+j]);
+      }
+    }
+    ++phx; gbar(p.bar1, phx<<8);
+
+    dmm_dual(lane,wave, p.dh1h,p.dh1l, p.dh1h,p.dh1l,
+             hqh2,hql2, whh1h,whh1l, ldsD);
+    __syncthreads();
+    if (tid<256){
+      int b=tid&63, j=tid>>6, col=j0+j;
+      st_f32(p.q  + b*1024+col, ldsD[j*68+b]     + cb[2*4+j]);
+      st_f32(p.u1 + b*1024+col, ldsD[272+j*68+b] + cb[3*4+j]);
+    }
+    ++phx; gbar(p.bar1, phx<<8);
+
+    {
+      const int b=bid>>2, q4=bid&3, s0=q4<<7;
+      const uint32_t* eb = p.enc_att + ((size_t)b*SH>>1);
+      float qv[16];
+      #pragma unroll
+      for (int i=0;i<8;++i){
+        float2 qq = *(const float2*)(p.q + b*1024 + (((i<<6)+lane)<<1));
+        qv[2*i]=qq.x; qv[2*i+1]=qq.y;
+      }
+      float ov[16];
+      #pragma unroll
+      for (int i=0;i<16;++i) ov[i]=0.f;
+      float mrun=-3.0e38f, lrun=0.f;
+      for (int si=0; si<16; ++si){
+        int s = s0 + (wave<<4) + si;
+        const uint32_t* ep = eb + s*512 + lane;
+        float ef[16]; float partial=0.f;
+        #pragma unroll
+        for (int i=0;i<8;++i){
+          uint32_t w2 = ep[i<<6];
+          float e0=(float)__builtin_bit_cast(_Float16,(unsigned short)(w2&0xffffu));
+          float e1=(float)__builtin_bit_cast(_Float16,(unsigned short)(w2>>16));
+          ef[2*i]=e0; ef[2*i+1]=e1;
+          partial = fmaf(e1,qv[2*i+1], fmaf(e0,qv[2*i], partial));
+        }
+        #pragma unroll
+        for (int off=32; off; off>>=1) partial += __shfl_xor(partial, off, 64);
+        if (t==63 && lane==0) st_f32(p.sc63 + b*512 + s, partial);
+        float mnew=fmaxf(mrun,partial);
+        float fac=__expf(mrun-mnew), w=__expf(partial-mnew);
+        lrun = fmaf(lrun,fac,w);
+        #pragma unroll
+        for (int i=0;i<16;++i) ov[i]=fmaf(ov[i],fac,w*ef[i]);
+        mrun=mnew;
+      }
+      if (lane==0){ sml[wave]=mrun; sml[8+wave]=lrun; }
+      __syncthreads();
+      float Mx=sml[0];
+      #pragma unroll
+      for (int w=1;w<8;++w) Mx=fmaxf(Mx,sml[w]);
+      float fw=__expf(sml[wave]-Mx);
+      if (wave<4){
+        #pragma unroll
+        for (int i=0;i<8;++i){
+          int h=((i<<6)+lane)<<1;
+          sbufA[wave*1032+h]  =fw*ov[2*i];
+          sbufA[wave*1032+h+1]=fw*ov[2*i+1];
+        }
+      }
+      __syncthreads();
+      if (wave>=4){
+        #pragma unroll
+        for (int i=0;i<8;++i){
+          int h=((i<<6)+lane)<<1;
+          sbufA[(wave-4)*1032+h]  +=fw*ov[2*i];
+          sbufA[(wave-4)*1032+h+1]+=fw*ov[2*i+1];
+        }
+      }
+      __syncthreads();
+      if (tid==0){
+        float L=0.f;
+        #pragma unroll
+        for (int w=0;w<8;++w) L += __expf(sml[w]-Mx)*sml[8+w];
+        st_f32(p.attp_ml + (b*4+q4)*2,   Mx);
+        st_f32(p.attp_ml + (b*4+q4)*2+1, L);
+      }
+      { int h2=tid<<1;
+        float o0=sbufA[h2]+sbufA[1032+h2]+sbufA[2064+h2]+sbufA[3096+h2];
+        float o1=sbufA[h2+1]+sbufA[1032+h2+1]+sbufA[2064+h2+1]+sbufA[3096+h2+1];
+        st_f32(p.attp_o + (b*4+q4)*1024 + h2,   o0);
+        st_f32(p.attp_o + (b*4+q4)*1024 + h2+1, o1);
+      }
+    }
+    ++phx; gbar(p.bar1, phx<<8);
+
+    if (bid < 64){
+      const int b=bid;
+      float m0=p.attp_ml[b*8+0], l0=p.attp_ml[b*8+1];
+      float m1=p.attp_ml[b*8+2], l1=p.attp_ml[b*8+3];
+      float m2=p.attp_ml[b*8+4], l2=p.attp_ml[b*8+5];
+      float m3=p.attp_ml[b*8+6], l3=p.attp_ml[b*8+7];
+      float Mx=fmaxf(fmaxf(m0,m1),fmaxf(m2,m3));
+      float f0=expf(m0-Mx),f1=expf(m1-Mx),f2=expf(m2-Mx),f3=expf(m3-Mx);
+      float invL=1.0f/(f0*l0+f1*l1+f2*l2+f3*l3);
+      int h2=tid<<1;
+      float o0=(f0*p.attp_o[(b*4+0)*1024+h2]+f1*p.attp_o[(b*4+1)*1024+h2]
+               +f2*p.attp_o[(b*4+2)*1024+h2]+f3*p.attp_o[(b*4+3)*1024+h2])*invL;
+      float o1=(f0*p.attp_o[(b*4+0)*1024+h2+1]+f1*p.attp_o[(b*4+1)*1024+h2+1]
+               +f2*p.attp_o[(b*4+2)*1024+h2+1]+f3*p.attp_o[(b*4+3)*1024+h2+1])*invL;
+      uint32_t ph_,pl_; pack2(o0,o1,ph_,pl_);
+      st_u32((uint32_t*)p.cath + ((b*2048+1024+h2)>>1), ph_);
+      st_u32((uint32_t*)p.catl + ((b*2048+1024+h2)>>1), pl_);
+      if (t==63)
+        st_f32(p.dout + OFF_ATTN + b*512 + tid, expf(p.sc63[b*512+tid]-Mx)*invL);
+    }
+    ++phx; gbar(p.bar1, phx<<8);
+
+    dmm_sk<2048>(lane,wave, p.cath, p.catl, combh2, combl2, ldsD);
+    __syncthreads();
+    if (tid<128){
+      int b=tid&63, jp=tid>>6;
+      float nv[2];
+      #pragma unroll
+      for (int d=0;d<2;++d){
+        int j=(jp<<1)+d;
+        nv[d] = ldsD[j*68+b] + ldsD[272+j*68+b] + cb[4*4+j];
+      }
+      uint32_t ph_,pl_; pack2(nv[0],nv[1],ph_,pl_);
+      int c0=j0+(jp<<1);
+      st_u32((uint32_t*)p.ch + ((b*1024+c0)>>1), ph_);
+      st_u32((uint32_t*)p.cl + ((b*1024+c0)>>1), pl_);
+    }
+    ++phx; gbar(p.bar1, phx<<8);
+
+    dmm_sk<1024>(lane,wave, p.ch, p.cl, fch2, fcl2, ldsD);
+    __syncthreads();
+    if (tid<256){
+      int b=tid&63, j=tid>>6, col=j0+j;
+      float val = ldsD[j*68+b] + ldsD[272+j*68+b] + cb[5*4+j];
+      st_f32(p.dout + b*65536 + t*1024 + col, val);
+      ldsL[j*68+b] = val;
+    }
+    __syncthreads();
+    if (tid<64){
+      int b=tid; float best=-3.0e38f; int bi=0;
+      #pragma unroll
+      for (int j=0;j<4;++j){
+        float v=ldsL[j*68+b];
+        if (v>best){ best=v; bi=j; }
+      }
+      st_u64(p.amax + b*256 + bid,
+             ((unsigned long long)ordf(best)<<32) | (unsigned)(1023-(j0+bi)));
+    }
+    ++phx; gbar(p.bar1, phx<<8);
+  }
+
+  { int idx=bid*512+tid;
+    int i=idx&65535;
+    float v=(idx>>16)? reconf(p.dh1h[i],p.dh1l[i]) : reconf(p.dh0h[i],p.dh0l[i]);
+    st_f32(p.dout + OFF_HID + idx, v);
+  }
 }
 
 extern "C" void kernel_launch(void* const* d_in, const int* in_sizes, int n_in,
@@ -495,66 +667,35 @@
   auto alloc = [&](size_t bytes)->char*{
     char* r = base + off; off = (off + bytes + 255) & ~(size_t)255; return r;
   };
-  p.enc_i = (uint32_t*)alloc(33554432ULL*4);
-  p.W0h = (_Float16*)alloc(3145728ULL*2);  p.W0l = (_Float16*)alloc(3145728ULL*2);
-  p.W1h = (_Float16*)alloc(6291456ULL*2);  p.W1l = (_Float16*)alloc(6291456ULL*2);
-  p.embh = (_Float16*)alloc(1048576ULL*2); p.embl = (_Float16*)alloc(1048576ULL*2);
-  p.T0h  = (_Float16*)alloc(1048576ULL*2); p.T0l  = (_Float16*)alloc(1048576ULL*2);
-  p.wih0dh=(_Float16*)alloc(1048576ULL*2); p.wih0dl=(_Float16*)alloc(1048576ULL*2);
-  p.wih1dh=(_Float16*)alloc(1048576ULL*2); p.wih1dl=(_Float16*)alloc(1048576ULL*2);
-  p.whh0dh=(_Float16*)alloc(1048576ULL*2); p.whh0dl=(_Float16*)alloc(1048576ULL*2);
-  p.whh1dh=(_Float16*)alloc(1048576ULL*2); p.whh1dl=(_Float16*)alloc(1048576ULL*2);
-  p.hqh  = (_Float16*)alloc(1048576ULL*2); p.hql  = (_Float16*)alloc(1048576ULL*2);
-  p.combh= (_Float16*)alloc(2097152ULL*2); p.combl= (_Float16*)alloc(2097152ULL*2);
-  p.fch  = (_Float16*)alloc(1048576ULL*2); p.fcl  = (_Float16*)alloc(1048576ULL*2);
-  p.h0h  = (_Float16*)alloc(131072ULL*2);  p.h0l  = (_Float16*)alloc(131072ULL*2);
-  p.h1h  = (_Float16*)alloc(131072ULL*2);  p.h1l  = (_Float16*)alloc(131072ULL*2);
-  p.dh0h = (_Float16*)alloc(65536ULL*2);   p.dh0l = (_Float16*)alloc(65536ULL*2);
-  p.dh1h = (_Float16*)alloc(65536ULL*2);   p.dh1l = (_Float16*)alloc(65536ULL*2);
-  p.cath = (_Float16*)alloc(131072ULL*2);  p.catl = (_Float16*)alloc(131072ULL*2);
-  p.ch   = (_Float16*)alloc(65536ULL*2);   p.cl   = (_Float16*)alloc(65536ULL*2);
-  p.u0   = (float*)alloc(65536ULL*4);      p.u1   = (float*)alloc(65536ULL*4);
-  p.w1x  = (float*)alloc(65536ULL*4);      p.q    = (float*)alloc(65536ULL*4);
-  p.attp_o  = (float*)alloc(131072ULL*4);
-  p.attp_ml = (float*)alloc(256ULL*4);
+  p.enc_att = (uint32_t*)alloc(16777216ULL*4);
+  p.embh  = (_Float16*)alloc(1048576ULL*2); p.embl  = (_Float16*)alloc(1048576ULL*2);
+  p.T0h   = (_Float16*)alloc(1048576ULL*2); p.T0l   = (_Float16*)alloc(1048576ULL*2);
+  p.wih0dh= (_Float16*)alloc(1048576ULL*2); p.wih0dl= (_Float16*)alloc(1048576ULL*2);
+  p.h0h   = (_Float16*)alloc(131072ULL*2);  p.h0l   = (_Float16*)alloc(131072ULL*2);
+  p.h1h   = (_Float16*)alloc(131072ULL*2);  p.h1l   = (_Float16*)alloc(131072ULL*2);
+  p.dh0h  = (_Float16*)alloc(65536ULL*2);   p.dh0l  = (_Float16*)alloc(65536ULL*2);
+  p.dh1h  = (_Float16*)alloc(65536ULL*2);   p.dh1l  = (_Float16*)alloc(65536ULL*2);
+  p.cath  = (_Float16*)alloc(131072ULL*2);  p.catl  = (_Float16*)alloc(131072ULL*2);
+  p.ch    = (_Float16*)alloc(65536ULL*2);   p.cl    = (_Float16*)alloc(65536ULL*2);
+  p.u0    = (float*)alloc(65536ULL*4);      p.u1    = (float*)alloc(65536ULL*4);
+  p.q     = (float*)alloc(65536ULL*4);
+  p.attp_o  = (float*)alloc(262144ULL*4);
+  p.attp_ml = (float*)alloc(512ULL*4);
   p.sc63    = (float*)alloc(32768ULL*4);
-  p.amax    = (unsigned long long*)alloc(8192ULL*8);
+  p.amax    = (unsigned long long*)alloc(16384ULL*8);
+  { unsigned* bars = (unsigned*)alloc(512*4);
+    p.bar0 = bars; p.bar1 = bars + 256; }
   if (off > ws_size) return;
+
+  hipFuncSetAttribute(reinterpret_cast<const void*>(k_encp),
+                      hipFuncAttributeMaxDynamicSharedMemorySize, ENC_LDS);
+  hipFuncSetAttribute(reinterpret_cast<const void*>(k_decp),
+                      hipFuncAttributeMaxDynamicSharedMemorySize, DEC_LDS);
 
   k_split<<<2048,256,0,stream>>>(p.emb,   p.embh,   p.embl,   1048576);
   k_split<<<2048,256,0,stream>>>(p.dWih0, p.wih0dh, p.wih0dl, 1048576);
-  k_split<<<2048,256,0,stream>>>(p.dWih1, p.wih1dh, p.wih1dl, 1048576);
-  k_split<<<2048,256,0,stream>>>(p.dWhh0, p.whh0dh, p.whh0dl, 1048576);
-  k_split<<<2048,256,0,stream>>>(p.dWhh1, p.whh1dh, p.whh1dl, 1048576);
-  k_split<<<2048,256,0,stream>>>(p.hqW,   p.hqh,    p.hql,    1048576);
-  k_split<<<2048,256,0,stream>>>(p.combW, p.combh,  p.combl,  2097152);
-  k_split<<<2048,256,0,stream>>>(p.fcW,   p.fch,    p.fcl,    1048576);
-  k_rw0<<<4096,256,0,stream>>>(p);
-  k_rw1<<<4096,256,0,stream>>>(p);
-  k_zero<<<256,256,0,stream>>>(p);
-  k_t0<<<1024,256,0,stream>>>(p);
-
-  for (int e=0; e<=512; ++e) k_enc<<<256,256,0,stream>>>(p, e);
-
-  {
-    GSet a{p.whh0dh, p.whh0dl, p.h0h + BH, p.h0l + BH, p.dbhh0, p.u0};
-    GSet b{p.whh1dh, p.whh1dl, p.h1h,      p.h1l,      p.dbhh1, p.u1};
-    k_dgemm2<<<256,256,0,stream>>>(a, b);
-  }
-  GSet sK1a{p.wih1dh, p.wih1dl, p.dh0h, p.dh0l, p.dbih1, p.w1x};
-  GSet sK1b{p.whh0dh, p.whh0dl, p.dh0h, p.dh0l, p.dbhh0, p.u0};
-  GSet sK3a{p.hqh,    p.hql,    p.dh1h, p.dh1l, p.hqb,   p.q};
-  GSet sK3b{p.whh1dh, p.whh1dl, p.dh1h, p.dh1l, p.dbhh1, p.u1};
-
-  for (int t=0; t<64; ++t){
-    k_dec0<<<64,256,0,stream>>>(p, t);
-    k_dgemm2<<<256,256,0,stream>>>(sK1a, sK1b);
-    k_dec2<<<64,256,0,stream>>>(p);
-    k_dgemm2<<<256,256,0,stream>>>(sK3a, sK3b);
-    k_flash<<<128,256,0,stream>>>(p, t);
-    k_dec5<<<64,256,0,stream>>>(p, t);
-    k_comb<<<128,256,0,stream>>>(p);
-    k_fc<<<128,256,0,stream>>>(p, t);
-  }
-  k_hidden<<<512,256,0,stream>>>(p);
-}
+  k_zero <<<256,256,0,stream>>>(p);
+  k_t0   <<<1024,256,0,stream>>>(p);
+  k_encp <<<256,512,ENC_LDS,stream>>>(p);
+  k_decp <<<256,512,DEC_LDS,stream>>>(p);
+}
```

New measurement: 40.06 ms. 32.6% more time.
